# Optimization experiments

Measured on AMD Instinct MI355X. Metric: run time of the kernel, lower is better.

Reference implementation:

```python
import jax, jax.numpy as jnp
import numpy as np

B, T, C = 4, 2048, 1024
H = 16
D = C // H  # head_dim = 64


def setup_inputs() -> dict:
    key = jax.random.key(0)
    k1, k2, k3 = jax.random.split(key, 3)
    x = jax.random.normal(k1, (B, T, C), dtype=jnp.float32)
    # torch nn.Linear weight layout: [out_features, in_features]; y = x @ W.T
    w_attn = jax.random.normal(k2, (3 * C, C), dtype=jnp.float32) * (1.0 / np.sqrt(C))
    w_proj = jax.random.normal(k3, (C, C), dtype=jnp.float32) * (1.0 / np.sqrt(C))
    return {"x": x, "w_attn": w_attn, "w_proj": w_proj}


def _attention(x, w_attn, w_proj):
    qkv = jnp.einsum('btc,fc->btf', x, w_attn)           # [B,T,3C]
    q, k, v = jnp.split(qkv, 3, axis=-1)
    # [B,T,C] -> [B,H,T,D]
    q = q.reshape(B, T, H, D).transpose(0, 2, 1, 3)
    k = k.reshape(B, T, H, D).transpose(0, 2, 1, 3)
    v = v.reshape(B, T, H, D).transpose(0, 2, 1, 3)
    att = jnp.einsum('bhqd,bhkd->bhqk', q, k) * (1.0 / np.sqrt(D))
    causal = jnp.tril(jnp.ones((T, T), dtype=bool))      # [T,T]
    att = jnp.where(causal[None, None], att, -jnp.inf)
    att = jax.nn.softmax(att, axis=-1)
    out = jnp.einsum('bhqk,bhkd->bhqd', att, v)          # [B,H,T,D]
    out = out.transpose(0, 2, 1, 3).reshape(B, T, C)
    return jnp.einsum('btc,fc->btf', out, w_proj)        # [B,T,C]


def reference(x, w_attn, w_proj):
    return _attention(x, w_attn, w_proj)
```

## Files before the change

kernel.cpp:

```cpp
#include <hip/hip_runtime.h>
#include <hip/hip_bf16.h>

typedef __attribute__((ext_vector_type(8))) short s8b;
typedef __attribute__((ext_vector_type(4))) float f4;
typedef unsigned short u16;

union U8 { s8b v; unsigned long long u[2]; };

__device__ __forceinline__ u16 f2bf(float f) {
  union { float f; unsigned u; } x; x.f = f;
  unsigned r = x.u + 0x7fffu + ((x.u >> 16) & 1u);
  return (u16)(r >> 16);
}

__device__ __forceinline__ float exp2a(float x) {
  float r;
  asm("v_exp_f32 %0, %1" : "=v"(r) : "v"(x));
  return r;
}

__device__ __forceinline__ void gload16(const void* g, void* l) {
  __builtin_amdgcn_global_load_lds(
      (const __attribute__((address_space(1))) void*)g,
      (__attribute__((address_space(3))) void*)l, 16, 0, 0);
}

__global__ void cvt3_kernel(const float* __restrict__ x, const float* __restrict__ wa,
                            const float* __restrict__ wp, u16* __restrict__ xb,
                            u16* __restrict__ wab, u16* __restrict__ wpb) {
  const int i = blockIdx.x * blockDim.x + threadIdx.x;
  const float4* src;
  ushort4* dst;
  int idx;
  if (i < 2097152) { src = (const float4*)x; dst = (ushort4*)xb; idx = i; }
  else if (i < 2883584) { src = (const float4*)wa; dst = (ushort4*)wab; idx = i - 2097152; }
  else { src = (const float4*)wp; dst = (ushort4*)wpb; idx = i - 2883584; }
  const float4 v = src[idx];
  ushort4 o;
  o.x = f2bf(v.x); o.y = f2bf(v.y); o.z = f2bf(v.z); o.w = f2bf(v.w);
  dst[idx] = o;
}

#define BMT 128
#define BNT 128
#define BKT 64

template<int MODE, int TILES>
__global__ __launch_bounds__(256, 2)
void gemm_bt(const u16* __restrict__ A, const u16* __restrict__ Bm,
             float* __restrict__ Cf,
             u16* __restrict__ qo, u16* __restrict__ ko, u16* __restrict__ vo,
             int N, int K, int GX) {
  __shared__ u16 lds[2][2][BMT * BKT];
  const int tid = threadIdx.x;
  const int lane = tid & 63;
  const int w = tid >> 6;
  const int wr = w >> 1, wc = w & 1;
  const int ric = lane >> 3;
  const int ssw = (lane & 7) ^ ric;

  auto tile_ptrs = [&](int t, const u16*& Ab, const u16*& Bb, int& bm, int& bn) {
    const int d = blockIdx.x + t * gridDim.x;
    const int xcd = d & 7, ib = d >> 3;
    bm = xcd * 8 + (ib & 7);
    bn = ib >> 3;
    Ab = A + (size_t)bm * BMT * K;
    Bb = Bm + (size_t)bn * BNT * K;
  };

  const int nk = K / BKT;
  const u16 *Ab, *Bb, *AbN, *BbN;
  int bm, bn, bmN, bnN;
  tile_ptrs(0, Ab, Bb, bm, bn);

  {
#pragma unroll
    for (int c = 0; c < 4; ++c) {
      const int rch = w * 32 + c * 8;
      gload16(Ab + (size_t)(rch + ric) * K + ssw * 8, &lds[0][0][rch * BKT]);
      gload16(Bb + (size_t)(rch + ric) * K + ssw * 8, &lds[0][1][rch * BKT]);
    }
  }
  __syncthreads();

  for (int t = 0; t < TILES; ++t) {
    if (t + 1 < TILES) tile_ptrs(t + 1, AbN, BbN, bmN, bnN);
    f4 acc[4][4] = {};

    for (int kt = 0; kt < nk; kt += 2) {
#pragma unroll
      for (int h = 0; h < 2; ++h) {
        const int ktg = kt + h;
        {
          const u16* sA;
          const u16* sB;
          int ko_;
          bool do_stage = true;
          if (ktg + 1 < nk) { sA = Ab; sB = Bb; ko_ = (ktg + 1) * BKT; }
          else if (t + 1 < TILES) { sA = AbN; sB = BbN; ko_ = 0; }
          else do_stage = false;
          if (do_stage) {
#pragma unroll
            for (int c = 0; c < 4; ++c) {
              const int rch = w * 32 + c * 8;
              gload16(sA + (size_t)(rch + ric) * K + ko_ + ssw * 8, &lds[h ^ 1][0][rch * BKT]);
              gload16(sB + (size_t)(rch + ric) * K + ko_ + ssw * 8, &lds[h ^ 1][1][rch * BKT]);
            }
          }
        }
        const u16* At = &lds[h][0][0];
        const u16* Bt = &lds[h][1][0];
#pragma unroll
        for (int kk = 0; kk < 2; ++kk) {
          s8b a[4], b[4];
#pragma unroll
          for (int m = 0; m < 4; ++m) {
            const int row = wr * 64 + m * 16 + (lane & 15);
            a[m] = *(const s8b*)(At + row * BKT + ((((kk << 2) + (lane >> 4)) ^ (row & 7)) << 3));
          }
#pragma unroll
          for (int n = 0; n < 4; ++n) {
            const int row = wc * 64 + n * 16 + (lane & 15);
            b[n] = *(const s8b*)(Bt + row * BKT + ((((kk << 2) + (lane >> 4)) ^ (row & 7)) << 3));
          }
#pragma unroll
          for (int m = 0; m < 4; ++m)
#pragma unroll
            for (int n = 0; n < 4; ++n)
              acc[m][n] = __builtin_amdgcn_mfma_f32_16x16x32_bf16(a[m], b[n], acc[m][n], 0, 0, 0);
        }
        __syncthreads();
      }
    }

    if (MODE == 0) {
#pragma unroll
      for (int n = 0; n < 4; ++n) {
        const int f = bn * BNT + wc * 64 + n * 16 + (lane & 15);
        const int which = f >> 10;
        const int rem = f & 1023;
        const int h = rem >> 6, dd = rem & 63;
        if (which == 2) {
#pragma unroll
          for (int m = 0; m < 4; ++m) {
            const int i0 = bm * BMT + wr * 64 + m * 16 + (lane >> 4) * 4;
            const int bb = i0 >> 11, t0 = i0 & 2047;
            ushort4 pk;
            pk.x = f2bf(acc[m][n][0]);
            pk.y = f2bf(acc[m][n][1]);
            pk.z = f2bf(acc[m][n][2]);
            pk.w = f2bf(acc[m][n][3]);
            *(ushort4*)(&vo[((size_t)((bb << 4) + h) * 64 + dd) * 2048 + t0]) = pk;
          }
        } else {
          u16* dst = which == 0 ? qo : ko;
          const float sc = which == 0 ? 0.18033688f : 1.0f;
#pragma unroll
          for (int m = 0; m < 4; ++m) {
#pragma unroll
            for (int j = 0; j < 4; ++j) {
              const int i = bm * BMT + wr * 64 + m * 16 + (lane >> 4) * 4 + j;
              const int bb = i >> 11, tt = i & 2047;
              dst[((size_t)((bb << 4) + h) * 2048 + tt) * 64 + dd] = f2bf(acc[m][n][j] * sc);
            }
          }
        }
      }
    } else {
#pragma unroll
      for (int m = 0; m < 4; ++m) {
#pragma unroll
        for (int j = 0; j < 4; ++j) {
          const int i = bm * BMT + wr * 64 + m * 16 + (lane >> 4) * 4 + j;
#pragma unroll
          for (int n = 0; n < 4; ++n) {
            const int f = bn * BNT + wc * 64 + n * 16 + (lane & 15);
            Cf[(size_t)i * N + f] = acc[m][n][j];
          }
        }
      }
    }

    Ab = AbN; Bb = BbN; bm = bmN; bn = bnN;
  }
}

__global__ __launch_bounds__(256, 3)
void attn_kernel(const u16* __restrict__ q, const u16* __restrict__ k,
                 const u16* __restrict__ vt, u16* __restrict__ ao) {
  __shared__ u16 Kl[64 * 64];
  __shared__ u16 VTl[64 * 64];
  __shared__ u16 Pl[4][16 * 64];
  const int tid = threadIdx.x, lane = tid & 63, w = tid >> 6;
  const int dd = blockIdx.x;
  const int xcd = dd & 7, ib = dd >> 3;
  const int bh = xcd * 8 + (ib & 7);
  const int j4 = ib >> 3;
  const int s4 = j4 >> 2, r4 = j4 & 3;
  const int qi = (s4 == 0) ? 15 - r4 : (s4 == 1) ? 8 + r4 : (s4 == 2) ? 7 - r4 : r4;
  const int b = bh >> 4, h16 = bh & 15;
  const size_t hb = (size_t)bh * 2048 * 64;
  const int qlo = lane & 15, hi = lane >> 4;
  const int r0 = tid >> 3, sl = tid & 7;
  u16* pw = &Pl[w][0];

  const s8b ones = {16256, 16256, 16256, 16256, 16256, 16256, 16256, 16256};

  const u16* kp = k + hb + (size_t)r0 * 64 + sl * 8;
  const u16* vp = vt + hb + (size_t)r0 * 2048 + sl * 8;
  s8b kr[2], vr[2];
  auto load_regs = [&]() {
    kr[0] = *(const s8b*)kp;
    kr[1] = *(const s8b*)(kp + 32 * 64);
    vr[0] = *(const s8b*)vp;
    vr[1] = *(const s8b*)(vp + 32 * 2048);
    kp += 64 * 64;
    vp += 64;
  };
  auto write_lds = [&]() {
#pragma unroll
    for (int c0 = 0; c0 < 2; ++c0) {
      const int r = r0 + c0 * 32;
      const int off = r * 64 + ((sl ^ (r & 7) ^ (r >> 3)) << 3);
      *(s8b*)(&Kl[off]) = kr[c0];
      *(s8b*)(&VTl[off]) = vr[c0];
    }
  };

  auto softpack = [&](f4 (&s)[4], U8 (&pf)[2]) {
#pragma unroll
    for (int n = 0; n < 4; ++n)
#pragma unroll
      for (int j = 0; j < 4; ++j) s[n][j] = exp2a(s[n][j]);
#pragma unroll
    for (int n = 0; n < 4; ++n) {
      __hip_bfloat162 h0 = __float22bfloat162_rn(make_float2(s[n][0], s[n][1]));
      __hip_bfloat162 h1 = __float22bfloat162_rn(make_float2(s[n][2], s[n][3]));
      unsigned lo, hi2;
      __builtin_memcpy(&lo, &h0, 4);
      __builtin_memcpy(&hi2, &h1, 4);
      const unsigned long long w64 =
          (unsigned long long)lo | ((unsigned long long)hi2 << 32);
      const int cw = ((n << 2) + hi) ^ qlo;
      *(unsigned long long*)(pw + (qlo << 6) + (cw << 2)) = w64;
    }
#pragma unroll
    for (int kk = 0; kk < 2; ++kk) {
      const int ca = ((kk << 3) + (hi << 1)) ^ qlo;
      pf[kk].u[0] = *(const unsigned long long*)(pw + (qlo << 6) + (ca << 2));
      pf[kk].u[1] = *(const unsigned long long*)(pw + (qlo << 6) + ((ca ^ 1) << 2));
    }
  };

  const int nkt = 2 * qi + 2;
  s8b qf[2][2];
#pragma unroll
  for (int g = 0; g < 2; ++g) {
    const u16* qp = q + hb + (size_t)(qi * 128 + w * 32 + g * 16 + qlo) * 64 + hi * 8;
    qf[g][0] = *(const s8b*)qp;
    qf[g][1] = *(const s8b*)(qp + 32);
  }
  f4 acc0[5] = {}, acc1[5] = {};

  load_regs();
  write_lds();
  __syncthreads();

  for (int kt = 0; kt < nkt; ++kt) {
    const bool pf_next = (kt + 1 < nkt);
    if (pf_next) load_regs();

    f4 s0[4], s1[4];
#pragma unroll
    for (int n = 0; n < 4; ++n) {
      s0[n] = (f4){-64.f, -64.f, -64.f, -64.f};
      s1[n] = (f4){-64.f, -64.f, -64.f, -64.f};
    }
    __builtin_amdgcn_s_setprio(1);
#pragma unroll
    for (int n = 0; n < 4; ++n) {
      const int row = n * 16 + qlo;
      const int swz = (row & 7) ^ (row >> 3);
#pragma unroll
      for (int kk = 0; kk < 2; ++kk) {
        const s8b kf = *(const s8b*)(&Kl[row * 64 + ((((kk << 2) + hi) ^ swz) << 3)]);
        s0[n] = __builtin_amdgcn_mfma_f32_16x16x32_bf16(kf, qf[0][kk], s0[n], 0, 0, 0);
        s1[n] = __builtin_amdgcn_mfma_f32_16x16x32_bf16(kf, qf[1][kk], s1[n], 0, 0, 0);
      }
    }
    __builtin_amdgcn_s_setprio(0);

    const int dmb = (2 * qi - kt) * 64;
    if (dmb < 64) {
      const int thr0 = w * 32 + qlo + dmb;
      const int thr1 = thr0 + 16;
#pragma unroll
      for (int n = 0; n < 4; ++n)
#pragma unroll
        for (int j = 0; j < 4; ++j) {
          const int kidx = n * 16 + hi * 4 + j;
          if (kidx > thr0) s0[n][j] = -1e30f;
          if (kidx > thr1) s1[n][j] = -1e30f;
        }
    }

    U8 pf0[2], pf1[2];
    softpack(s0, pf0);
    softpack(s1, pf1);

    __builtin_amdgcn_s_setprio(1);
#pragma unroll
    for (int dn = 0; dn < 4; ++dn) {
      const int vrow = dn * 16 + qlo;
      const int vswz = (vrow & 7) ^ (vrow >> 3);
#pragma unroll
      for (int kk = 0; kk < 2; ++kk) {
        const s8b vf = *(const s8b*)(&VTl[vrow * 64 + ((((kk << 2) + hi) ^ vswz) << 3)]);
        acc0[dn] = __builtin_amdgcn_mfma_f32_16x16x32_bf16(pf0[kk].v, vf, acc0[dn], 0, 0, 0);
        acc1[dn] = __builtin_amdgcn_mfma_f32_16x16x32_bf16(pf1[kk].v, vf, acc1[dn], 0, 0, 0);
      }
    }
#pragma unroll
    for (int kk = 0; kk < 2; ++kk) {
      acc0[4] = __builtin_amdgcn_mfma_f32_16x16x32_bf16(pf0[kk].v, ones, acc0[4], 0, 0, 0);
      acc1[4] = __builtin_amdgcn_mfma_f32_16x16x32_bf16(pf1[kk].v, ones, acc1[4], 0, 0, 0);
    }
    __builtin_amdgcn_s_setprio(0);

    __syncthreads();
    if (pf_next) {
      write_lds();
      __syncthreads();
    }
  }

#pragma unroll
  for (int g = 0; g < 2; ++g) {
    const f4* accg = g ? acc1 : acc0;
#pragma unroll
    for (int j = 0; j < 4; ++j) {
      const float rl = 1.0f / accg[4][j];
      const int t = qi * 128 + w * 32 + g * 16 + hi * 4 + j;
#pragma unroll
      for (int dn = 0; dn < 4; ++dn) {
        const int dcol = dn * 16 + qlo;
        ao[((size_t)(b * 2048 + t)) * 1024 + h16 * 64 + dcol] = f2bf(accg[dn][j] * rl);
      }
    }
  }
}

extern "C" void kernel_launch(void* const* d_in, const int* in_sizes, int n_in,
                              void* d_out, int out_size, void* d_ws, size_t ws_size,
                              hipStream_t stream) {
  const float* x = (const float*)d_in[0];
  const float* w_attn = (const float*)d_in[1];
  const float* w_proj = (const float*)d_in[2];
  float* out = (float*)d_out;
  char* ws = (char*)d_ws;

  u16* xb  = (u16*)(ws);
  u16* wab = (u16*)(ws + (16u << 20));
  u16* wpb = (u16*)(ws + (22u << 20));
  u16* qb  = (u16*)(ws + (24u << 20));
  u16* kb  = (u16*)(ws + (40u << 20));
  u16* vb  = (u16*)(ws + (56u << 20));
  u16* ao  = xb;

  cvt3_kernel<<<12288, 256, 0, stream>>>(x, w_attn, w_proj, xb, wab, wpb);

  gemm_bt<0, 3><<<512, 256, 0, stream>>>(xb, wab, nullptr, qb, kb, vb,
                                         3072, 1024, 24);
  attn_kernel<<<1024, 256, 0, stream>>>(qb, kb, vb, ao);
  gemm_bt<1, 1><<<512, 256, 0, stream>>>(ao, wpb, out, nullptr, nullptr, nullptr,
                                         1024, 1024, 8);
}
```

Baseline: 137.7 us.

## Replace double-buffered LDS pipeline with single buffer in GEMM

The GEMM kernel drops its two-stage LDS double buffer for a single buffer. Each k-step now computes, synchronizes, stages the next tile and synchronizes again. This halves shared memory per block, which may allow more resident blocks. In exchange, global-to-LDS loads no longer overlap with MFMA compute and each k-step needs an extra barrier.

After: 146.7 us. 1.07x slower.

```diff
diff --git a/kernel.cpp b/kernel.cpp
--- a/kernel.cpp
+++ b/kernel.cpp
@@ -51,7 +51,7 @@
              float* __restrict__ Cf,
              u16* __restrict__ qo, u16* __restrict__ ko, u16* __restrict__ vo,
              int N, int K, int GX) {
-  __shared__ u16 lds[2][2][BMT * BKT];
+  __shared__ u16 lds[2][BMT * BKT];
   const int tid = threadIdx.x;
   const int lane = tid & 63;
   const int w = tid >> 6;
@@ -68,67 +68,56 @@
     Bb = Bm + (size_t)bn * BNT * K;
   };
 
+  auto stage = [&](const u16* Ab, const u16* Bb, int kt) {
+    const int ko_ = kt * BKT;
+#pragma unroll
+    for (int c = 0; c < 4; ++c) {
+      const int rch = w * 32 + c * 8;
+      gload16(Ab + (size_t)(rch + ric) * K + ko_ + ssw * 8, &lds[0][rch * BKT]);
+      gload16(Bb + (size_t)(rch + ric) * K + ko_ + ssw * 8, &lds[1][rch * BKT]);
+    }
+  };
+
   const int nk = K / BKT;
   const u16 *Ab, *Bb, *AbN, *BbN;
   int bm, bn, bmN, bnN;
   tile_ptrs(0, Ab, Bb, bm, bn);
-
-  {
-#pragma unroll
-    for (int c = 0; c < 4; ++c) {
-      const int rch = w * 32 + c * 8;
-      gload16(Ab + (size_t)(rch + ric) * K + ssw * 8, &lds[0][0][rch * BKT]);
-      gload16(Bb + (size_t)(rch + ric) * K + ssw * 8, &lds[0][1][rch * BKT]);
-    }
-  }
+  stage(Ab, Bb, 0);
   __syncthreads();
 
   for (int t = 0; t < TILES; ++t) {
     if (t + 1 < TILES) tile_ptrs(t + 1, AbN, BbN, bmN, bnN);
     f4 acc[4][4] = {};
 
-    for (int kt = 0; kt < nk; kt += 2) {
-#pragma unroll
-      for (int h = 0; h < 2; ++h) {
-        const int ktg = kt + h;
-        {
-          const u16* sA;
-          const u16* sB;
-          int ko_;
-          bool do_stage = true;
-          if (ktg + 1 < nk) { sA = Ab; sB = Bb; ko_ = (ktg + 1) * BKT; }
-          else if (t + 1 < TILES) { sA = AbN; sB = BbN; ko_ = 0; }
-          else do_stage = false;
-          if (do_stage) {
-#pragma unroll
-            for (int c = 0; c < 4; ++c) {
-              const int rch = w * 32 + c * 8;
-              gload16(sA + (size_t)(rch + ric) * K + ko_ + ssw * 8, &lds[h ^ 1][0][rch * BKT]);
-              gload16(sB + (size_t)(rch + ric) * K + ko_ + ssw * 8, &lds[h ^ 1][1][rch * BKT]);
-            }
-          }
-        }
-        const u16* At = &lds[h][0][0];
-        const u16* Bt = &lds[h][1][0];
-#pragma unroll
-        for (int kk = 0; kk < 2; ++kk) {
-          s8b a[4], b[4];
-#pragma unroll
-          for (int m = 0; m < 4; ++m) {
-            const int row = wr * 64 + m * 16 + (lane & 15);
-            a[m] = *(const s8b*)(At + row * BKT + ((((kk << 2) + (lane >> 4)) ^ (row & 7)) << 3));
-          }
-#pragma unroll
-          for (int n = 0; n < 4; ++n) {
-            const int row = wc * 64 + n * 16 + (lane & 15);
-            b[n] = *(const s8b*)(Bt + row * BKT + ((((kk << 2) + (lane >> 4)) ^ (row & 7)) << 3));
-          }
-#pragma unroll
-          for (int m = 0; m < 4; ++m)
-#pragma unroll
-            for (int n = 0; n < 4; ++n)
-              acc[m][n] = __builtin_amdgcn_mfma_f32_16x16x32_bf16(a[m], b[n], acc[m][n], 0, 0, 0);
-        }
+    for (int kt = 0; kt < nk; ++kt) {
+      const u16* At = &lds[0][0];
+      const u16* Bt = &lds[1][0];
+#pragma unroll
+      for (int kk = 0; kk < 2; ++kk) {
+        s8b a[4], b[4];
+#pragma unroll
+        for (int m = 0; m < 4; ++m) {
+          const int row = wr * 64 + m * 16 + (lane & 15);
+          a[m] = *(const s8b*)(At + row * BKT + ((((kk << 2) + (lane >> 4)) ^ (row & 7)) << 3));
+        }
+#pragma unroll
+        for (int n = 0; n < 4; ++n) {
+          const int row = wc * 64 + n * 16 + (lane & 15);
+          b[n] = *(const s8b*)(Bt + row * BKT + ((((kk << 2) + (lane >> 4)) ^ (row & 7)) << 3));
+        }
+#pragma unroll
+        for (int m = 0; m < 4; ++m)
+#pragma unroll
+          for (int n = 0; n < 4; ++n)
+            acc[m][n] = __builtin_amdgcn_mfma_f32_16x16x32_bf16(a[m], b[n], acc[m][n], 0, 0, 0);
+      }
+      __syncthreads();
+
+      if (kt + 1 < nk) {
+        stage(Ab, Bb, kt + 1);
+        __syncthreads();
+      } else if (t + 1 < TILES) {
+        stage(AbN, BbN, 0);
         __syncthreads();
       }
     }
```
